# Kernel tuning notes

Hardware: AMD Instinct MI355X
Metric: run time of the kernel (lower is better)

Reference implementation:

```python
import jax, jax.numpy as jnp
import numpy as np

B, D, T = 16384, 1024, 128  # batch, embed_dim, num_degradation_types
V, L = 4, 3                 # variants per sample, degradations per variant


def setup_inputs() -> dict:
    key = jax.random.key(0)
    k1, k2, k3, k4 = jax.random.split(key, 4)
    clean_embeddings = jax.random.normal(k1, (B, D), dtype=jnp.float32)
    W = jax.random.normal(k2, (T, D), dtype=jnp.float32) * (1.0 / np.sqrt(D))
    b = jnp.zeros((T,), dtype=jnp.float32)
    deg_indices = jax.random.randint(k3, (B, V, L), 0, T, dtype=jnp.int32)
    deg_mask = jax.random.randint(k4, (B, V, L), 0, 2, dtype=jnp.int32)
    return {"clean_embeddings": clean_embeddings, "W": W, "b": b,
            "deg_indices": deg_indices, "deg_mask": deg_mask}


def reference(clean_embeddings, W, b, deg_indices, deg_mask):
    # Linear + softmax: [B, T]
    logits = jnp.einsum("bd,td->bt", clean_embeddings, W) + b
    probs = jax.nn.softmax(logits, axis=-1)
    # Gather probs at each (batch, label) pair: [B, V*L] -> [B, V, L]
    flat_idx = deg_indices.reshape(B, V * L)
    gathered = jnp.take_along_axis(probs, flat_idx, axis=1).reshape(B, V, L)
    # Masked sum over all labels of a sample, divided by max(num_variants, 1)=V
    per_sample = (gathered * deg_mask.astype(probs.dtype)).sum(axis=(1, 2)) / V
    return per_sample.sum() / B
```

## Files before the change

### kernel.cpp

```cpp
#include <hip/hip_runtime.h>

#define B_SIZE 16384
#define D_DIM  1024
#define T_DIM  128
#define VLn    12
#define BM     32
#define BK     256
#define NCHUNK 4
#define NTHR   512
#define GRID   (B_SIZE / BM)
#define AROWF  258
#define AROWB  1032
#define ABUFB  (BM * AROWB)
#define SLSTR  132

typedef _Float16 half8  __attribute__((ext_vector_type(8)));
typedef __fp16   fp16x2 __attribute__((ext_vector_type(2)));
typedef float    f32x4  __attribute__((ext_vector_type(4)));

union Pack16 { fp16x2 h[4]; uint4 u; half8 v; };
union Frag   { uint4 u; half8 h; };

__device__ __forceinline__ uint4 pack8u(float4 v0, float4 v1) {
    Pack16 un;
    un.h[0] = __builtin_amdgcn_cvt_pkrtz(v0.x, v0.y);
    un.h[1] = __builtin_amdgcn_cvt_pkrtz(v0.z, v0.w);
    un.h[2] = __builtin_amdgcn_cvt_pkrtz(v1.x, v1.y);
    un.h[3] = __builtin_amdgcn_cvt_pkrtz(v1.z, v1.w);
    return un.u;
}
__device__ __forceinline__ half8 pack8f(const float* fp) {
    const float2 a = ((const float2*)fp)[0];
    const float2 b = ((const float2*)fp)[1];
    const float2 c = ((const float2*)fp)[2];
    const float2 d = ((const float2*)fp)[3];
    Pack16 un;
    un.h[0] = __builtin_amdgcn_cvt_pkrtz(a.x, a.y);
    un.h[1] = __builtin_amdgcn_cvt_pkrtz(b.x, b.y);
    un.h[2] = __builtin_amdgcn_cvt_pkrtz(c.x, c.y);
    un.h[3] = __builtin_amdgcn_cvt_pkrtz(d.x, d.y);
    return un.v;
}

__device__ __forceinline__ void dma16(const float* g, void* l) {
    __builtin_amdgcn_global_load_lds(
        (__attribute__((address_space(1))) void*)g,
        (__attribute__((address_space(3))) void*)l, 16, 0, 0);
}

__global__ __launch_bounds__(256)
void conv_w(const float* __restrict__ W, uint4* __restrict__ Wf,
            float* __restrict__ out) {
    if (blockIdx.x == 0 && threadIdx.x == 0) out[0] = 0.0f;
    const int j    = blockIdx.x * 256 + threadIdx.x;
    const int kc   = j >> 10;
    const int r    = j & 1023;
    const int g    = r >> 6;
    const int lane = r & 63;
    const int n = (g & 7) * 16 + (lane & 15);
    const int k = kc * 64 + (g >> 3) * 32 + ((lane >> 4) << 3);
    const float* src = W + (size_t)n * D_DIM + k;
    Wf[j] = pack8u(*(const float4*)src, *(const float4*)(src + 4));
}

__global__ __launch_bounds__(NTHR, 4)
void qloss_kernel(const float* __restrict__ emb,
                  const uint4* __restrict__ Wf,
                  const float* __restrict__ bias,
                  const int*   __restrict__ didx,
                  const int*   __restrict__ dmsk,
                  float*       __restrict__ out)
{
    __shared__ __align__(16) unsigned char smem[2 * ABUFB + 64];
    float* sL   = (float*)smem;
    float* sRed = (float*)(smem + 2 * ABUFB);

    const int t    = threadIdx.x;
    const int w    = t >> 6;
    const int lane = t & 63;
    const int m15  = lane & 15;
    const int quad = lane >> 4;
    const int r0   = blockIdx.x * BM;

    const float* aG0 = emb + (size_t)(r0 + 4 * w) * D_DIM + lane * 4;

    const int rg  = w >> 2;
    const int CT0 = 2 * (w & 3);

    const uint4* bP = Wf + lane;

    f32x4 acc[2];
    acc[0] = (f32x4){0.f, 0.f, 0.f, 0.f};
    acc[1] = (f32x4){0.f, 0.f, 0.f, 0.f};

    Frag bp[3][2];

#define LOADB(s, slot)                                                        \
    do {                                                                      \
        bp[slot][0].u = bP[(size_t)((s) >> 1) * 1024 +                        \
                           (((s) & 1) * 8 + CT0 + 0) * 64];                   \
        bp[slot][1].u = bP[(size_t)((s) >> 1) * 1024 +                        \
                           (((s) & 1) * 8 + CT0 + 1) * 64];                   \
    } while (0)

#pragma unroll
    for (int r = 0; r < 4; ++r)
        dma16(aG0 + (size_t)r * D_DIM, smem + (4 * w + r) * AROWB);
    LOADB(0, 0);
    LOADB(1, 1);
    asm volatile("s_waitcnt vmcnt(4)" ::: "memory");
    __builtin_amdgcn_sched_barrier(0);
    __builtin_amdgcn_s_barrier();
    __builtin_amdgcn_sched_barrier(0);

#pragma unroll
    for (int kc = 0; kc < NCHUNK; ++kc) {
        const float* bufC = (const float*)(smem + (kc & 1) * ABUFB);
        unsigned char* bufN = (unsigned char*)smem + ((kc & 1) ^ 1) * ABUFB;

        if (kc + 1 < NCHUNK) {
#pragma unroll
            for (int r = 0; r < 4; ++r)
                dma16(aG0 + (size_t)r * D_DIM + (kc + 1) * BK,
                      bufN + (4 * w + r) * AROWB);
        }

#pragma unroll
        for (int ks = 0; ks < 8; ++ks) {
            const int s = kc * 8 + ks;
            if (s + 2 < 32) LOADB(s + 2, (s + 2) % 3);
            const float* fp = bufC + (16 * rg + m15) * AROWF + ks * 32 + quad * 8;
            const half8 a = pack8f(fp);
            acc[0] = __builtin_amdgcn_mfma_f32_16x16x32_f16(a, bp[s % 3][0].h, acc[0], 0, 0, 0);
            acc[1] = __builtin_amdgcn_mfma_f32_16x16x32_f16(a, bp[s % 3][1].h, acc[1], 0, 0, 0);
        }

        if (kc + 1 < NCHUNK) {
            asm volatile("s_waitcnt vmcnt(4)" ::: "memory");
            __builtin_amdgcn_sched_barrier(0);
            __builtin_amdgcn_s_barrier();
            __builtin_amdgcn_sched_barrier(0);
        }
    }
#undef LOADB

    __syncthreads();
    const float b0v = bias[CT0 * 16 + m15];
    const float b1v = bias[(CT0 + 1) * 16 + m15];
#pragma unroll
    for (int i = 0; i < 4; ++i) {
        const int row = 16 * rg + quad * 4 + i;
        sL[row * SLSTR + CT0 * 16 + m15]       = acc[0][i] + b0v;
        sL[row * SLSTR + (CT0 + 1) * 16 + m15] = acc[1][i] + b1v;
    }
    __syncthreads();

    {
        const int row = t >> 4, s = t & 15;
        float* base = &sL[row * SLSTR + s * 8];
        float v[8];
        *(float4*)&v[0] = *(const float4*)(base);
        *(float4*)&v[4] = *(const float4*)(base + 4);
        float m = -1e30f;
#pragma unroll
        for (int j = 0; j < 8; ++j) m = fmaxf(m, v[j]);
#pragma unroll
        for (int off = 1; off < 16; off <<= 1) m = fmaxf(m, __shfl_xor(m, off));
        float ssum = 0.f;
#pragma unroll
        for (int j = 0; j < 8; ++j) { v[j] = __expf(v[j] - m); ssum += v[j]; }
#pragma unroll
        for (int off = 1; off < 16; off <<= 1) ssum += __shfl_xor(ssum, off);
        const float inv = 1.0f / ssum;
#pragma unroll
        for (int j = 0; j < 8; ++j) v[j] *= inv;
        *(float4*)(base)     = *(const float4*)&v[0];
        *(float4*)(base + 4) = *(const float4*)&v[4];
    }
    __syncthreads();

    float p = 0.f;
    if (t < BM * VLn) {
        const int gi  = r0 * VLn + t;
        const int row = t / VLn;
        const int idx = didx[gi];
        const int mk  = dmsk[gi];
        p = mk ? sL[row * SLSTR + idx] : 0.f;
    }
#pragma unroll
    for (int off = 1; off < 64; off <<= 1) p += __shfl_xor(p, off);
    if (lane == 0) sRed[w] = p;
    __syncthreads();
    if (t == 0) {
        float s = 0.f;
#pragma unroll
        for (int i = 0; i < 8; ++i) s += sRed[i];
        atomicAdd(out, s * (1.0f / 65536.0f));
    }
}

extern "C" void kernel_launch(void* const* d_in, const int* in_sizes, int n_in,
                              void* d_out, int out_size, void* d_ws, size_t ws_size,
                              hipStream_t stream) {
    const float* emb  = (const float*)d_in[0];
    const float* W    = (const float*)d_in[1];
    const float* bias = (const float*)d_in[2];
    const int*   didx = (const int*)d_in[3];
    const int*   dmsk = (const int*)d_in[4];
    float* out = (float*)d_out;

    uint4* Wf = (uint4*)d_ws;

    conv_w<<<64, 256, 0, stream>>>(W, Wf, out);
    qloss_kernel<<<GRID, NTHR, 0, stream>>>(emb, Wf, bias, didx, dmsk, out);
}
```

Baseline: 112.0 us.

## Deepen to 4-stage LDS pipeline with B staged via DMA and 64-row tiles

Doubles the row tile to 64 and splits K into 16 chunks of 64, staging both embedding rows (via 4-byte global_load_lds) and the pre-converted fp16 weight fragments into a 4-deep LDS ring with 3 chunks in flight. Each wave now computes 4 column tiles instead of 2, reusing each A fragment across more MFMAs, and B is read from LDS instead of per-lane register prefetch from global. The aim is more memory-level parallelism and less per-block overhead. In exchange, LDS use and launch bounds rise so occupancy drops to 2 blocks per CU, and 4-byte DMA issues many more load instructions.

```diff
diff --git a/kernel.cpp b/kernel.cpp
--- a/kernel.cpp
+++ b/kernel.cpp
@@ -4,14 +4,15 @@
 #define D_DIM  1024
 #define T_DIM  128
 #define VLn    12
-#define BM     32
-#define BK     256
-#define NCHUNK 4
+#define BM     64
+#define BKF    64
+#define NCHUNK 16
 #define NTHR   512
 #define GRID   (B_SIZE / BM)
-#define AROWF  258
-#define AROWB  1032
-#define ABUFB  (BM * AROWB)
+#define AROWB  264
+#define ACHB   (BM * AROWB)
+#define BCHB   16384
+#define PAIRB  (ACHB + BCHB)
 #define SLSTR  132
 
 typedef _Float16 half8  __attribute__((ext_vector_type(8)));
@@ -42,11 +43,19 @@
     return un.v;
 }
 
-__device__ __forceinline__ void dma16(const float* g, void* l) {
+__device__ __forceinline__ void dma16(const uint4* g, void* l) {
     __builtin_amdgcn_global_load_lds(
-        (__attribute__((address_space(1))) void*)g,
+        (const __attribute__((address_space(1))) void*)g,
         (__attribute__((address_space(3))) void*)l, 16, 0, 0);
 }
+__device__ __forceinline__ void dma4(const float* g, void* l) {
+    __builtin_amdgcn_global_load_lds(
+        (const __attribute__((address_space(1))) void*)g,
+        (__attribute__((address_space(3))) void*)l, 4, 0, 0);
+}
+
+#define WAITV(n) asm volatile("s_waitcnt vmcnt(" #n ")" ::: "memory")
+#define SB0()    __builtin_amdgcn_sched_barrier(0)
 
 __global__ __launch_bounds__(256)
 void conv_w(const float* __restrict__ W, uint4* __restrict__ Wf,
@@ -63,7 +72,7 @@
     Wf[j] = pack8u(*(const float4*)src, *(const float4*)(src + 4));
 }
 
-__global__ __launch_bounds__(NTHR, 4)
+__global__ __launch_bounds__(NTHR, 2)
 void qloss_kernel(const float* __restrict__ emb,
                   const uint4* __restrict__ Wf,
                   const float* __restrict__ bias,
@@ -71,9 +80,9 @@
                   const int*   __restrict__ dmsk,
                   float*       __restrict__ out)
 {
-    __shared__ __align__(16) unsigned char smem[2 * ABUFB + 64];
+    __shared__ __align__(16) unsigned char smem[4 * PAIRB + 64];
     float* sL   = (float*)smem;
-    float* sRed = (float*)(smem + 2 * ABUFB);
+    float* sRed = (float*)(smem + 4 * PAIRB);
 
     const int t    = threadIdx.x;
     const int w    = t >> 6;
@@ -82,110 +91,111 @@
     const int quad = lane >> 4;
     const int r0   = blockIdx.x * BM;
 
-    const float* aG0 = emb + (size_t)(r0 + 4 * w) * D_DIM + lane * 4;
-
-    const int rg  = w >> 2;
-    const int CT0 = 2 * (w & 3);
-
-    const uint4* bP = Wf + lane;
-
-    f32x4 acc[2];
-    acc[0] = (f32x4){0.f, 0.f, 0.f, 0.f};
-    acc[1] = (f32x4){0.f, 0.f, 0.f, 0.f};
-
-    Frag bp[3][2];
-
-#define LOADB(s, slot)                                                        \
-    do {                                                                      \
-        bp[slot][0].u = bP[(size_t)((s) >> 1) * 1024 +                        \
-                           (((s) & 1) * 8 + CT0 + 0) * 64];                   \
-        bp[slot][1].u = bP[(size_t)((s) >> 1) * 1024 +                        \
-                           (((s) & 1) * 8 + CT0 + 1) * 64];                   \
-    } while (0)
-
-#pragma unroll
-    for (int r = 0; r < 4; ++r)
-        dma16(aG0 + (size_t)r * D_DIM, smem + (4 * w + r) * AROWB);
-    LOADB(0, 0);
-    LOADB(1, 1);
-    asm volatile("s_waitcnt vmcnt(4)" ::: "memory");
-    __builtin_amdgcn_sched_barrier(0);
-    __builtin_amdgcn_s_barrier();
-    __builtin_amdgcn_sched_barrier(0);
-
-#pragma unroll
-    for (int kc = 0; kc < NCHUNK; ++kc) {
-        const float* bufC = (const float*)(smem + (kc & 1) * ABUFB);
-        unsigned char* bufN = (unsigned char*)smem + ((kc & 1) ^ 1) * ABUFB;
-
-        if (kc + 1 < NCHUNK) {
-#pragma unroll
-            for (int r = 0; r < 4; ++r)
-                dma16(aG0 + (size_t)r * D_DIM + (kc + 1) * BK,
-                      bufN + (4 * w + r) * AROWB);
+    const int rr = w & 3;
+    const int cg = w >> 2;
+
+    const float* aS = emb + (size_t)(r0 + 8 * w) * D_DIM + lane;
+    const uint4* bS = Wf + 2 * w * 64 + lane;
+
+    f32x4 acc[4];
+#pragma unroll
+    for (int ct = 0; ct < 4; ++ct) acc[ct] = (f32x4){0.f, 0.f, 0.f, 0.f};
+
+    auto issue = [&](int j) {
+        unsigned char* Ab = smem + (j & 3) * PAIRB;
+#pragma unroll
+        for (int r = 0; r < 8; ++r)
+            dma4(aS + (size_t)r * D_DIM + j * BKF, Ab + (8 * w + r) * AROWB);
+        unsigned char* Bb = Ab + ACHB;
+        dma16(bS + (size_t)j * 1024,      Bb + (2 * w) * 1024);
+        dma16(bS + (size_t)j * 1024 + 64, Bb + (2 * w + 1) * 1024);
+    };
+
+    auto compute = [&](int kc) {
+        const unsigned char* pb = smem + (kc & 3) * PAIRB;
+        const float* Af = (const float*)pb;
+        const uint4* Bf = (const uint4*)(pb + ACHB);
+#pragma unroll
+        for (int st = 0; st < 2; ++st) {
+            const float* fp = Af + (16 * rr + m15) * (AROWB / 4) + st * 32 + quad * 8;
+            const half8 a = pack8f(fp);
+#pragma unroll
+            for (int ct = 0; ct < 4; ++ct) {
+                Frag b;
+                b.u = Bf[(st * 8 + 4 * cg + ct) * 64 + lane];
+                acc[ct] = __builtin_amdgcn_mfma_f32_16x16x32_f16(a, b.h, acc[ct], 0, 0, 0);
+            }
         }
-
-#pragma unroll
-        for (int ks = 0; ks < 8; ++ks) {
-            const int s = kc * 8 + ks;
-            if (s + 2 < 32) LOADB(s + 2, (s + 2) % 3);
-            const float* fp = bufC + (16 * rg + m15) * AROWF + ks * 32 + quad * 8;
-            const half8 a = pack8f(fp);
-            acc[0] = __builtin_amdgcn_mfma_f32_16x16x32_f16(a, bp[s % 3][0].h, acc[0], 0, 0, 0);
-            acc[1] = __builtin_amdgcn_mfma_f32_16x16x32_f16(a, bp[s % 3][1].h, acc[1], 0, 0, 0);
+    };
+
+    issue(0); issue(1); issue(2);
+
+#pragma unroll
+    for (int kc = 0; kc < NCHUNK - 3; ++kc) {
+        WAITV(20);
+        SB0();
+        __builtin_amdgcn_s_barrier();
+        SB0();
+        issue(kc + 3);
+        SB0();
+        compute(kc);
+    }
+    WAITV(20); SB0(); __builtin_amdgcn_s_barrier(); SB0(); compute(13);
+    WAITV(10); SB0(); __builtin_amdgcn_s_barrier(); SB0(); compute(14);
+    WAITV(0);  SB0(); __builtin_amdgcn_s_barrier(); SB0(); compute(15);
+
+    __syncthreads();
+    float bv[4];
+#pragma unroll
+    for (int ct = 0; ct < 4; ++ct) bv[ct] = bias[(4 * cg + ct) * 16 + m15];
+#pragma unroll
+    for (int i = 0; i < 4; ++i) {
+        const int row = 16 * rr + quad * 4 + i;
+#pragma unroll
+        for (int ct = 0; ct < 4; ++ct)
+            sL[row * SLSTR + (4 * cg + ct) * 16 + m15] = acc[ct][i] + bv[ct];
+    }
+    __syncthreads();
+
+    {
+        const int row = t >> 3, sub = t & 7;
+        float* base = &sL[row * SLSTR + sub * 16];
+        float v[16];
+        *(float4*)&v[0]  = *(const float4*)(base);
+        *(float4*)&v[4]  = *(const float4*)(base + 4);
+        *(float4*)&v[8]  = *(const float4*)(base + 8);
+        *(float4*)&v[12] = *(const float4*)(base + 12);
+        float m = -1e30f;
+#pragma unroll
+        for (int j = 0; j < 16; ++j) m = fmaxf(m, v[j]);
+#pragma unroll
+        for (int off = 1; off < 8; off <<= 1) m = fmaxf(m, __shfl_xor(m, off));
+        float ssum = 0.f;
+#pragma unroll
+        for (int j = 0; j < 16; ++j) { v[j] = __expf(v[j] - m); ssum += v[j]; }
+#pragma unroll
+        for (int off = 1; off < 8; off <<= 1) ssum += __shfl_xor(ssum, off);
+        const float inv = 1.0f / ssum;
+#pragma unroll
+        for (int j = 0; j < 16; ++j) v[j] *= inv;
+        *(float4*)(base)      = *(const float4*)&v[0];
+        *(float4*)(base + 4)  = *(const float4*)&v[4];
+        *(float4*)(base + 8)  = *(const float4*)&v[8];
+        *(float4*)(base + 12) = *(const float4*)&v[12];
+    }
+    __syncthreads();
+
+    float p = 0.f;
+#pragma unroll
+    for (int e = 0; e < 2; ++e) {
+        const int item = e * 512 + t;
+        if (item < BM * VLn) {
+            const int gi  = r0 * VLn + item;
+            const int row = item / VLn;
+            const int mk  = dmsk[gi];
+            const int idx = didx[gi];
+            if (mk) p += sL[row * SLSTR + idx];
         }
-
-        if (kc + 1 < NCHUNK) {
-            asm volatile("s_waitcnt vmcnt(4)" ::: "memory");
-            __builtin_amdgcn_sched_barrier(0);
-            __builtin_amdgcn_s_barrier();
-            __builtin_amdgcn_sched_barrier(0);
-        }
-    }
-#undef LOADB
-
-    __syncthreads();
-    const float b0v = bias[CT0 * 16 + m15];
-    const float b1v = bias[(CT0 + 1) * 16 + m15];
-#pragma unroll
-    for (int i = 0; i < 4; ++i) {
-        const int row = 16 * rg + quad * 4 + i;
-        sL[row * SLSTR + CT0 * 16 + m15]       = acc[0][i] + b0v;
-        sL[row * SLSTR + (CT0 + 1) * 16 + m15] = acc[1][i] + b1v;
-    }
-    __syncthreads();
-
-    {
-        const int row = t >> 4, s = t & 15;
-        float* base = &sL[row * SLSTR + s * 8];
-        float v[8];
-        *(float4*)&v[0] = *(const float4*)(base);
-        *(float4*)&v[4] = *(const float4*)(base + 4);
-        float m = -1e30f;
-#pragma unroll
-        for (int j = 0; j < 8; ++j) m = fmaxf(m, v[j]);
-#pragma unroll
-        for (int off = 1; off < 16; off <<= 1) m = fmaxf(m, __shfl_xor(m, off));
-        float ssum = 0.f;
-#pragma unroll
-        for (int j = 0; j < 8; ++j) { v[j] = __expf(v[j] - m); ssum += v[j]; }
-#pragma unroll
-        for (int off = 1; off < 16; off <<= 1) ssum += __shfl_xor(ssum, off);
-        const float inv = 1.0f / ssum;
-#pragma unroll
-        for (int j = 0; j < 8; ++j) v[j] *= inv;
-        *(float4*)(base)     = *(const float4*)&v[0];
-        *(float4*)(base + 4) = *(const float4*)&v[4];
-    }
-    __syncthreads();
-
-    float p = 0.f;
-    if (t < BM * VLn) {
-        const int gi  = r0 * VLn + t;
-        const int row = t / VLn;
-        const int idx = didx[gi];
-        const int mk  = dmsk[gi];
-        p = mk ? sL[row * SLSTR + idx] : 0.f;
     }
 #pragma unroll
     for (int off = 1; off < 64; off <<= 1) p += __shfl_xor(p, off);
```

Result: no change. 113.4 us (+1.2%).

## Halve block to four waves, each computing two row tiles reusing W fragments

Applied to the files above, without the earlier changes.

The block shrinks from 8 waves to 4. Each wave now covers all 32 rows as two 16-row MFMA tiles and two column tiles, so each loaded W fragment feeds twice as many MFMAs. Each wave's DMA share of embedding rows doubles, and softmax and the gather epilogue are remapped to 256 threads. The aim is to cut redundant W register loads and per-block overhead, but it halves the resident waves per CU available to hide global-load latency.

```diff
diff --git a/kernel.cpp b/kernel.cpp
--- a/kernel.cpp
+++ b/kernel.cpp
@@ -7,7 +7,7 @@
 #define BM     32
 #define BK     256
 #define NCHUNK 4
-#define NTHR   512
+#define NTHR   256
 #define GRID   (B_SIZE / BM)
 #define AROWF  258
 #define AROWB  1032
@@ -44,9 +44,12 @@
 
 __device__ __forceinline__ void dma16(const float* g, void* l) {
     __builtin_amdgcn_global_load_lds(
-        (__attribute__((address_space(1))) void*)g,
+        (const __attribute__((address_space(1))) void*)g,
         (__attribute__((address_space(3))) void*)l, 16, 0, 0);
 }
+
+#define WAITV(n) asm volatile("s_waitcnt vmcnt(" #n ")" ::: "memory")
+#define SB0()    __builtin_amdgcn_sched_barrier(0)
 
 __global__ __launch_bounds__(256)
 void conv_w(const float* __restrict__ W, uint4* __restrict__ Wf,
@@ -63,7 +66,7 @@
     Wf[j] = pack8u(*(const float4*)src, *(const float4*)(src + 4));
 }
 
-__global__ __launch_bounds__(NTHR, 4)
+__global__ __launch_bounds__(NTHR, 2)
 void qloss_kernel(const float* __restrict__ emb,
                   const uint4* __restrict__ Wf,
                   const float* __restrict__ bias,
@@ -71,7 +74,7 @@
                   const int*   __restrict__ dmsk,
                   float*       __restrict__ out)
 {
-    __shared__ __align__(16) unsigned char smem[2 * ABUFB + 64];
+    __shared__ __align__(16) unsigned char smem[2 * ABUFB + 32];
     float* sL   = (float*)smem;
     float* sRed = (float*)(smem + 2 * ABUFB);
 
@@ -82,16 +85,17 @@
     const int quad = lane >> 4;
     const int r0   = blockIdx.x * BM;
 
-    const float* aG0 = emb + (size_t)(r0 + 4 * w) * D_DIM + lane * 4;
-
-    const int rg  = w >> 2;
-    const int CT0 = 2 * (w & 3);
-
+    const float* aG0 = emb + (size_t)(r0 + 8 * w) * D_DIM + lane * 4;
+
+    const int CT0 = 2 * w;
     const uint4* bP = Wf + lane;
 
-    f32x4 acc[2];
-    acc[0] = (f32x4){0.f, 0.f, 0.f, 0.f};
-    acc[1] = (f32x4){0.f, 0.f, 0.f, 0.f};
+    f32x4 acc[2][2];
+#pragma unroll
+    for (int rt = 0; rt < 2; ++rt)
+#pragma unroll
+        for (int j = 0; j < 2; ++j)
+            acc[rt][j] = (f32x4){0.f, 0.f, 0.f, 0.f};
 
     Frag bp[3][2];
 
@@ -104,14 +108,14 @@
     } while (0)
 
 #pragma unroll
-    for (int r = 0; r < 4; ++r)
-        dma16(aG0 + (size_t)r * D_DIM, smem + (4 * w + r) * AROWB);
+    for (int r = 0; r < 8; ++r)
+        dma16(aG0 + (size_t)r * D_DIM, smem + (8 * w + r) * AROWB);
     LOADB(0, 0);
     LOADB(1, 1);
-    asm volatile("s_waitcnt vmcnt(4)" ::: "memory");
-    __builtin_amdgcn_sched_barrier(0);
+    WAITV(4);
+    SB0();
     __builtin_amdgcn_s_barrier();
-    __builtin_amdgcn_sched_barrier(0);
+    SB0();
 
 #pragma unroll
     for (int kc = 0; kc < NCHUNK; ++kc) {
@@ -120,26 +124,31 @@
 
         if (kc + 1 < NCHUNK) {
 #pragma unroll
-            for (int r = 0; r < 4; ++r)
+            for (int r = 0; r < 8; ++r)
                 dma16(aG0 + (size_t)r * D_DIM + (kc + 1) * BK,
-                      bufN + (4 * w + r) * AROWB);
+                      bufN + (8 * w + r) * AROWB);
         }
 
 #pragma unroll
         for (int ks = 0; ks < 8; ++ks) {
             const int s = kc * 8 + ks;
             if (s + 2 < 32) LOADB(s + 2, (s + 2) % 3);
-            const float* fp = bufC + (16 * rg + m15) * AROWF + ks * 32 + quad * 8;
-            const half8 a = pack8f(fp);
-            acc[0] = __builtin_amdgcn_mfma_f32_16x16x32_f16(a, bp[s % 3][0].h, acc[0], 0, 0, 0);
-            acc[1] = __builtin_amdgcn_mfma_f32_16x16x32_f16(a, bp[s % 3][1].h, acc[1], 0, 0, 0);
+            const float* fp0 = bufC + m15 * AROWF + ks * 32 + quad * 8;
+            const float* fp1 = fp0 + 16 * AROWF;
+            const half8 a0 = pack8f(fp0);
+            const half8 a1 = pack8f(fp1);
+            const int sl = s % 3;
+            acc[0][0] = __builtin_amdgcn_mfma_f32_16x16x32_f16(a0, bp[sl][0].h, acc[0][0], 0, 0, 0);
+            acc[0][1] = __builtin_amdgcn_mfma_f32_16x16x32_f16(a0, bp[sl][1].h, acc[0][1], 0, 0, 0);
+            acc[1][0] = __builtin_amdgcn_mfma_f32_16x16x32_f16(a1, bp[sl][0].h, acc[1][0], 0, 0, 0);
+            acc[1][1] = __builtin_amdgcn_mfma_f32_16x16x32_f16(a1, bp[sl][1].h, acc[1][1], 0, 0, 0);
         }
 
         if (kc + 1 < NCHUNK) {
-            asm volatile("s_waitcnt vmcnt(4)" ::: "memory");
-            __builtin_amdgcn_sched_barrier(0);
+            WAITV(4);
+            SB0();
             __builtin_amdgcn_s_barrier();
-            __builtin_amdgcn_sched_barrier(0);
+            SB0();
         }
     }
 #undef LOADB
@@ -148,55 +157,61 @@
     const float b0v = bias[CT0 * 16 + m15];
     const float b1v = bias[(CT0 + 1) * 16 + m15];
 #pragma unroll
-    for (int i = 0; i < 4; ++i) {
-        const int row = 16 * rg + quad * 4 + i;
-        sL[row * SLSTR + CT0 * 16 + m15]       = acc[0][i] + b0v;
-        sL[row * SLSTR + (CT0 + 1) * 16 + m15] = acc[1][i] + b1v;
+    for (int rt = 0; rt < 2; ++rt)
+#pragma unroll
+        for (int i = 0; i < 4; ++i) {
+            const int row = 16 * rt + quad * 4 + i;
+            sL[row * SLSTR + CT0 * 16 + m15]       = acc[rt][0][i] + b0v;
+            sL[row * SLSTR + (CT0 + 1) * 16 + m15] = acc[rt][1][i] + b1v;
+        }
+    __syncthreads();
+
+    {
+        const int row = t >> 3, sub = t & 7;
+        float* base = &sL[row * SLSTR + sub * 16];
+        float v[16];
+        *(float4*)&v[0]  = *(const float4*)(base);
+        *(float4*)&v[4]  = *(const float4*)(base + 4);
+        *(float4*)&v[8]  = *(const float4*)(base + 8);
+        *(float4*)&v[12] = *(const float4*)(base + 12);
+        float m = -1e30f;
+#pragma unroll
+        for (int j = 0; j < 16; ++j) m = fmaxf(m, v[j]);
+#pragma unroll
+        for (int off = 1; off < 8; off <<= 1) m = fmaxf(m, __shfl_xor(m, off));
+        float ssum = 0.f;
+#pragma unroll
+        for (int j = 0; j < 16; ++j) { v[j] = __expf(v[j] - m); ssum += v[j]; }
+#pragma unroll
+        for (int off = 1; off < 8; off <<= 1) ssum += __shfl_xor(ssum, off);
+        const float inv = 1.0f / ssum;
+#pragma unroll
+        for (int j = 0; j < 16; ++j) v[j] *= inv;
+        *(float4*)(base)      = *(const float4*)&v[0];
+        *(float4*)(base + 4)  = *(const float4*)&v[4];
+        *(float4*)(base + 8)  = *(const float4*)&v[8];
+        *(float4*)(base + 12) = *(const float4*)&v[12];
     }
     __syncthreads();
 
-    {
-        const int row = t >> 4, s = t & 15;
-        float* base = &sL[row * SLSTR + s * 8];
-        float v[8];
-        *(float4*)&v[0] = *(const float4*)(base);
-        *(float4*)&v[4] = *(const float4*)(base + 4);
-        float m = -1e30f;
-#pragma unroll
-        for (int j = 0; j < 8; ++j) m = fmaxf(m, v[j]);
-#pragma unroll
-        for (int off = 1; off < 16; off <<= 1) m = fmaxf(m, __shfl_xor(m, off));
-        float ssum = 0.f;
-#pragma unroll
-        for (int j = 0; j < 8; ++j) { v[j] = __expf(v[j] - m); ssum += v[j]; }
-#pragma unroll
-        for (int off = 1; off < 16; off <<= 1) ssum += __shfl_xor(ssum, off);
-        const float inv = 1.0f / ssum;
-#pragma unroll
-        for (int j = 0; j < 8; ++j) v[j] *= inv;
-        *(float4*)(base)     = *(const float4*)&v[0];
-        *(float4*)(base + 4) = *(const float4*)&v[4];
-    }
-    __syncthreads();
-
     float p = 0.f;
-    if (t < BM * VLn) {
-        const int gi  = r0 * VLn + t;
-        const int row = t / VLn;
-        const int idx = didx[gi];
-        const int mk  = dmsk[gi];
-        p = mk ? sL[row * SLSTR + idx] : 0.f;
+#pragma unroll
+    for (int e = 0; e < 2; ++e) {
+        const int item = e * 256 + t;
+        if (item < BM * VLn) {
+            const int gi  = r0 * VLn + item;
+            const int row = item / VLn;
+            const int mk  = dmsk[gi];
+            const int idx = didx[gi];
+            if (mk) p += sL[row * SLSTR + idx];
+        }
     }
 #pragma unroll
     for (int off = 1; off < 64; off <<= 1) p += __shfl_xor(p, off);
     if (lane == 0) sRed[w] = p;
     __syncthreads();
-    if (t == 0) {
-        float s = 0.f;
-#pragma unroll
-        for (int i = 0; i < 8; ++i) s += sRed[i];
-        atomicAdd(out, s * (1.0f / 65536.0f));
-    }
+    if (t == 0)
+        atomicAdd(out, (sRed[0] + sRed[1] + sRed[2] + sRed[3]) * (1.0f / 65536.0f));
 }
 
 extern "C" void kernel_launch(void* const* d_in, const int* in_sizes, int n_in,
```

New measurement: 108.9 us, median of 2. 2.8% less time.
